# Performance work log

Hardware: AMD Instinct MI355X
Metric: run time of the kernel (lower is better)

The kernel has to match this reference:

```python
import jax, jax.numpy as jnp
import numpy as np


def setup_inputs() -> dict:
    key = jax.random.key(0)
    ks = jax.random.split(key, 20)
    B, P, ENC = 128, 196, 512
    DEC, ATT, EMB, V, S1 = 512, 256, 256, 5000, 257
    s = 0.02
    inp = {
        "features": jax.random.normal(ks[0], (B, P, ENC), jnp.float32),
        "captions": jax.random.randint(ks[1], (B, S1), 0, V),
        "emb": jax.random.normal(ks[2], (V, EMB), jnp.float32) * s,
        "Ua_w": jax.random.normal(ks[3], (ENC, ATT), jnp.float32) * s,
        "Ua_b": jnp.zeros((ATT,), jnp.float32),
        "Wa_w": jax.random.normal(ks[4], (DEC, ATT), jnp.float32) * s,
        "Wa_b": jnp.zeros((ATT,), jnp.float32),
        "va_w": jax.random.normal(ks[5], (ATT,), jnp.float32) * s,
        "va_b": jnp.zeros((), jnp.float32),
        "ih_w": jax.random.normal(ks[6], (ENC, DEC), jnp.float32) * s,
        "ih_b": jnp.zeros((DEC,), jnp.float32),
        "ic_w": jax.random.normal(ks[7], (ENC, DEC), jnp.float32) * s,
        "ic_b": jnp.zeros((DEC,), jnp.float32),
        "W_ih": jax.random.normal(ks[8], (EMB + ENC, 4 * DEC), jnp.float32) * s,
        "b_ih": jnp.zeros((4 * DEC,), jnp.float32),
        "W_hh": jax.random.normal(ks[9], (DEC, 4 * DEC), jnp.float32) * s,
        "b_hh": jnp.zeros((4 * DEC,), jnp.float32),
        "fcn_w": jax.random.normal(ks[10], (DEC, V), jnp.float32) * s,
        "fcn_b": jnp.zeros((V,), jnp.float32),
    }
    return inp


def reference(features, captions, emb, Ua_w, Ua_b, Wa_w, Wa_b, va_w, va_b,
              ih_w, ih_b, ic_w, ic_b, W_ih, b_ih, W_hh, b_hh, fcn_w, fcn_b):
    # embeds: [B, S+1, E]; we consume embeds[:, :S]
    embeds = emb[captions]
    mean_f = features.mean(axis=1)                      # [B, ENC]
    h0 = mean_f @ ih_w + ih_b                           # [B, DEC]
    c0 = mean_f @ ic_w + ic_b
    Uf = features @ Ua_w + Ua_b                         # [B, P, ATT] precomputed

    def step(carry, x_emb):
        h, c = carry
        att = jnp.tanh(Uf + (h @ Wa_w + Wa_b)[:, None, :])   # [B, P, ATT]
        scores = att @ va_w + va_b                            # [B, P]
        alpha = jax.nn.softmax(scores, axis=1)
        context = jnp.einsum('bp,bpe->be', alpha, features)   # [B, ENC]
        x = jnp.concatenate([x_emb, context], axis=1)         # [B, EMB+ENC]
        gates = x @ W_ih + b_ih + h @ W_hh + b_hh             # [B, 4*DEC]
        i, f, g, o = jnp.split(gates, 4, axis=1)
        c = jax.nn.sigmoid(f) * c + jax.nn.sigmoid(i) * jnp.tanh(g)
        h = jax.nn.sigmoid(o) * jnp.tanh(c)
        out = h @ fcn_w + fcn_b                               # dropout is identity (p=0)
        return (h, c), out

    xs = jnp.swapaxes(embeds[:, :-1], 0, 1)             # [S, B, EMB]
    _, preds = jax.lax.scan(step, (h0, c0), xs)         # [S, B, V]
    return jnp.swapaxes(preds, 0, 1)                    # [B, S, V]
```

## Files before the change

kernel.cpp:

```cpp
#include <hip/hip_runtime.h>
#include <hip/hip_bf16.h>

#define B 128
#define P 196
#define PP 200
#define ENC 512
#define DEC 512
#define ATT 256
#define EMB 256
#define V 5000
#define S 256
#define S1 257
#define NG 2048
#define KS 16

typedef __attribute__((ext_vector_type(4))) short s4v;
typedef __attribute__((ext_vector_type(8))) short s8v;

__device__ __forceinline__ float bf2f(short u) {
    unsigned int x = ((unsigned int)(unsigned short)u) << 16;
    float f; __builtin_memcpy(&f, &x, 4); return f;
}

__device__ __forceinline__ float tanhf_fast(float x) {
    float xx = fminf(fmaxf(x, -15.f), 15.f);
    float t = __expf(2.f * xx);
    return (t - 1.f) * __builtin_amdgcn_rcpf(t + 1.f);
}

__global__ __launch_bounds__(256) void k_mean(const float* __restrict__ feat,
                                              float* __restrict__ mean_f) {
    int idx = blockIdx.x * 256 + threadIdx.x;
    int b = idx >> 9, e = idx & 511;
    const float* fp = feat + (size_t)b * P * ENC + e;
    float s = 0.f;
    for (int p = 0; p < P; ++p) s += fp[(size_t)p * ENC];
    mean_f[idx] = s * (1.0f / (float)P);
}

__global__ __launch_bounds__(256) void k_init_hc(const float* __restrict__ mean_f,
        const float* __restrict__ ih_w, const float* __restrict__ ih_b,
        const float* __restrict__ ic_w, const float* __restrict__ ic_b,
        float* __restrict__ h, float* __restrict__ c) {
    int idx = blockIdx.x * 256 + threadIdx.x;
    int b = idx >> 9, d = idx & 511;
    const float* mf = mean_f + (size_t)b * ENC;
    float sh = ih_b[d], sc = ic_b[d];
    for (int e = 0; e < ENC; ++e) {
        float m = mf[e];
        sh = fmaf(m, ih_w[(size_t)e * DEC + d], sh);
        sc = fmaf(m, ic_w[(size_t)e * DEC + d], sc);
    }
    h[idx] = sh; c[idx] = sc;
}

__global__ __launch_bounds__(256) void k_uf(const float* __restrict__ feat,
        const float* __restrict__ Ua_w, const float* __restrict__ Ua_b,
        __hip_bfloat16* __restrict__ Uf) {
    int row0 = blockIdx.x * 8;
    int a = threadIdx.x;
    __shared__ float fs[8][ENC];
    for (int i = threadIdx.x; i < 8 * ENC; i += 256) {
        int r = i >> 9, e = i & 511;
        fs[r][e] = feat[(size_t)(row0 + r) * ENC + e];
    }
    __syncthreads();
    float acc[8];
    float bia = Ua_b[a];
#pragma unroll
    for (int r = 0; r < 8; ++r) acc[r] = bia;
    for (int e = 0; e < ENC; ++e) {
        float w = Ua_w[(size_t)e * ATT + a];
#pragma unroll
        for (int r = 0; r < 8; ++r) acc[r] = fmaf(fs[r][e], w, acc[r]);
    }
#pragma unroll
    for (int r = 0; r < 8; ++r)
        Uf[(size_t)(row0 + r) * ATT + a] = __float2bfloat16(acc[r]);
}

__global__ __launch_bounds__(512) void k_featT(const float* __restrict__ feat,
        __hip_bfloat16* __restrict__ featT) {
    int b = blockIdx.x, p0 = blockIdx.y * 8;
    int e = threadIdx.x;
    __hip_bfloat16 v[8];
#pragma unroll
    for (int i = 0; i < 8; ++i) {
        int p = p0 + i;
        float f = (p < P) ? feat[((size_t)b * P + p) * ENC + e] : 0.f;
        v[i] = __float2bfloat16(f);
    }
    __builtin_memcpy(&featT[((size_t)b * ENC + e) * PP + p0], v, 16);
}

__global__ __launch_bounds__(256) void k_wacvt(const float* __restrict__ w,
        __hip_bfloat16* __restrict__ wb) {
    int i = blockIdx.x * 256 + threadIdx.x;
    wb[i] = __float2bfloat16(w[i]);
}

__global__ __launch_bounds__(256) void k_gemb(const float* __restrict__ emb,
        const int* __restrict__ captions, const float* __restrict__ W_ih,
        __hip_bfloat16* __restrict__ Gemb) {
    __shared__ float As[16][128];
    __shared__ float Bs[16][128];
    __shared__ int rowcap[128];
    int m0 = blockIdx.x * 128;
    int n0 = blockIdx.y * 128;
    int tid = threadIdx.x;
    if (tid < 128) {
        int m = m0 + tid;
        rowcap[tid] = captions[(size_t)(m & 127) * S1 + (m >> 7)];
    }
    __syncthreads();
    int tx = tid & 15, ty = tid >> 4;
    float acc[8][8];
#pragma unroll
    for (int i = 0; i < 8; ++i)
#pragma unroll
        for (int j = 0; j < 8; ++j) acc[i][j] = 0.f;
    int arow = tid >> 1, ak = (tid & 1) * 8;
    int bkk = tid >> 4, bn = (tid & 15) * 8;
    for (int k0 = 0; k0 < EMB; k0 += 16) {
        {
            const float* ap = emb + (size_t)rowcap[arow] * EMB + k0 + ak;
            float4 v0 = *(const float4*)ap;
            float4 v1 = *(const float4*)(ap + 4);
            As[ak + 0][arow] = v0.x; As[ak + 1][arow] = v0.y;
            As[ak + 2][arow] = v0.z; As[ak + 3][arow] = v0.w;
            As[ak + 4][arow] = v1.x; As[ak + 5][arow] = v1.y;
            As[ak + 6][arow] = v1.z; As[ak + 7][arow] = v1.w;
        }
        {
            const float* bp = W_ih + (size_t)(k0 + bkk) * NG + n0 + bn;
            *(float4*)&Bs[bkk][bn] = *(const float4*)bp;
            *(float4*)&Bs[bkk][bn + 4] = *(const float4*)(bp + 4);
        }
        __syncthreads();
#pragma unroll
        for (int kk = 0; kk < 16; ++kk) {
            float4 a0 = *(const float4*)&As[kk][ty * 8];
            float4 a1 = *(const float4*)&As[kk][ty * 8 + 4];
            float4 b0 = *(const float4*)&Bs[kk][tx * 8];
            float4 b1 = *(const float4*)&Bs[kk][tx * 8 + 4];
            float av[8] = {a0.x, a0.y, a0.z, a0.w, a1.x, a1.y, a1.z, a1.w};
            float bv[8] = {b0.x, b0.y, b0.z, b0.w, b1.x, b1.y, b1.z, b1.w};
#pragma unroll
            for (int i = 0; i < 8; ++i)
#pragma unroll
                for (int j = 0; j < 8; ++j)
                    acc[i][j] = fmaf(av[i], bv[j], acc[i][j]);
        }
        __syncthreads();
    }
#pragma unroll
    for (int i = 0; i < 8; ++i) {
        __hip_bfloat16* gp = Gemb + (size_t)(m0 + ty * 8 + i) * NG + n0 + tx * 8;
#pragma unroll
        for (int j = 0; j < 8; ++j) gp[j] = __float2bfloat16(acc[i][j]);
    }
}

__global__ __launch_bounds__(1024) void k_attn_cell(
        const float* __restrict__ partials, const __hip_bfloat16* __restrict__ Gemb,
        const float* __restrict__ b_ih, const float* __restrict__ b_hh,
        float* __restrict__ h, const float* __restrict__ cr, float* __restrict__ cw,
        float* __restrict__ Hall,
        const __hip_bfloat16* __restrict__ Wa_wb, const float* __restrict__ Wa_b,
        const __hip_bfloat16* __restrict__ Uf, const __hip_bfloat16* __restrict__ featT,
        const float* __restrict__ va_w, const float* __restrict__ va_b,
        float* __restrict__ ctxp, float* __restrict__ mlp,
        int t, int use_gemb, int use_hall) {
    int g = blockIdx.x;
    int b = g >> 1, half = g & 1;
    int tid = threadIdx.x;
    int base = half ? 96 : 0;
    int cnt  = half ? 100 : 96;
    __shared__ short ufs[100][ATT];
    __shared__ float hs[DEC];
    __shared__ float wahp[4][ATT];
    __shared__ float wahs[ATT];
    __shared__ float sc[104];
    __shared__ float red[4];
    __shared__ float cpart[2][ENC];

    if (tid < 512) {
        if (t > 0) {
            int d = tid;
            float s0 = b_ih[d]           + b_hh[d];
            float s1 = b_ih[d + DEC]     + b_hh[d + DEC];
            float s2 = b_ih[d + 2 * DEC] + b_hh[d + 2 * DEC];
            float s3 = b_ih[d + 3 * DEC] + b_hh[d + 3 * DEC];
#pragma unroll
            for (int ks = 0; ks < KS; ++ks) {
                const float* pp = partials + ((size_t)ks * B + b) * NG + d;
                s0 += pp[0]; s1 += pp[DEC]; s2 += pp[2 * DEC]; s3 += pp[3 * DEC];
            }
            if (use_gemb) {
                const __hip_bfloat16* gp = Gemb + ((size_t)(t - 1) * B + b) * NG + d;
                s0 += __bfloat162float(gp[0]);
                s1 += __bfloat162float(gp[DEC]);
                s2 += __bfloat162float(gp[2 * DEC]);
                s3 += __bfloat162float(gp[3 * DEC]);
            }
            size_t gidx = (size_t)b * DEC + d;
            float ii = 1.f / (1.f + __expf(-s0));
            float ff = 1.f / (1.f + __expf(-s1));
            float gg = tanhf_fast(s2);
            float oo = 1.f / (1.f + __expf(-s3));
            float cn = ff * cr[gidx] + ii * gg;
            float hn = oo * tanhf_fast(cn);
            hs[d] = hn;
            if (half == 0) {
                cw[gidx] = cn;
                h[gidx] = hn;
                if (use_hall) Hall[((size_t)(t - 1) * B + b) * DEC + d] = hn;
            }
        } else {
            hs[tid] = h[(size_t)b * DEC + tid];
        }
    } else if (t < S) {
        const __hip_bfloat16* ub = Uf + ((size_t)b * P + base) * ATT;
        for (int i = tid - 512; i < cnt * 32; i += 512) {
            int p = i >> 5, c = (i & 31) * 8;
            *(s8v*)&ufs[p][c] = *(const s8v*)(ub + (size_t)p * ATT + c);
        }
    }
    __syncthreads();
    if (t == S) return;

    {
        int a = tid & 255, q = tid >> 8;
        float acc = 0.f;
        const __hip_bfloat16* wp = Wa_wb + (size_t)(q * 128) * ATT + a;
        const float* hq = &hs[q * 128];
#pragma unroll 4
        for (int dd = 0; dd < 128; ++dd)
            acc = fmaf(hq[dd], bf2f(*(const short*)&wp[(size_t)dd * ATT]), acc);
        wahp[q][a] = acc;
    }
    __syncthreads();
    if (tid < ATT)
        wahs[tid] = Wa_b[tid] + wahp[0][tid] + wahp[1][tid] + wahp[2][tid] + wahp[3][tid];
    __syncthreads();

    {
        int w = tid >> 6, lane = tid & 63;
        float4 wv = *(const float4*)&wahs[lane * 4];
        float4 vv = *(const float4*)&va_w[lane * 4];
        float vb = va_b[0];
        for (int pl = w; pl < cnt; pl += 16) {
            s4v u4 = *(const s4v*)&ufs[pl][lane * 4];
            float ssc = vv.x * tanhf_fast(bf2f(u4.x) + wv.x)
                      + vv.y * tanhf_fast(bf2f(u4.y) + wv.y)
                      + vv.z * tanhf_fast(bf2f(u4.z) + wv.z)
                      + vv.w * tanhf_fast(bf2f(u4.w) + wv.w);
#pragma unroll
            for (int off = 32; off; off >>= 1) ssc += __shfl_down(ssc, off);
            if (lane == 0) sc[pl] = ssc + vb;
        }
    }
    __syncthreads();

    {
        int lane = tid & 63;
        float v = (tid < cnt) ? sc[tid] : -1e30f;
        if (tid < 128) {
            float m = v;
#pragma unroll
            for (int off = 32; off; off >>= 1) m = fmaxf(m, __shfl_down(m, off));
            if (lane == 0) red[tid >> 6] = m;
        }
        __syncthreads();
        float mh = fmaxf(red[0], red[1]);
        float e = (tid < cnt) ? __expf(v - mh) : 0.f;
        if (tid < 128) {
            float l = e;
#pragma unroll
            for (int off = 32; off; off >>= 1) l += __shfl_down(l, off);
            if (lane == 0) red[2 + (tid >> 6)] = l;
        }
        __syncthreads();
        if (tid < cnt) sc[tid] = e;
        else if (tid < 104) sc[tid] = 0.f;
        if (tid == 0) {
            mlp[((size_t)half * B + b) * 2 + 0] = mh;
            mlp[((size_t)half * B + b) * 2 + 1] = red[2] + red[3];
        }
    }
    __syncthreads();

    {
        int e = tid & 511, ph = tid >> 9;
        int start = half ? (ph ? 7 : 0) : (ph ? 6 : 0);
        int nch   = half ? (ph ? 6 : 7) : 6;
        float acc = 0.f;
        const __hip_bfloat16* fr = featT + ((size_t)b * ENC + e) * PP + base + start * 8;
        for (int ch = 0; ch < nch; ++ch) {
            s8v raw = *(const s8v*)(fr + ch * 8);
            const float* sp = &sc[(start + ch) * 8];
#pragma unroll
            for (int j = 0; j < 8; ++j)
                acc = fmaf(sp[j], bf2f(raw[j]), acc);
        }
        cpart[ph][e] = acc;
    }
    __syncthreads();
    if (tid < ENC)
        ctxp[((size_t)half * B + b) * ENC + tid] = cpart[0][tid] + cpart[1][tid];
}

__global__ __launch_bounds__(256) void k_gates(const float* __restrict__ emb,
        const int* __restrict__ captions, int t,
        const float* __restrict__ ctxp, const float* __restrict__ mlp,
        const float* __restrict__ h,
        const float* __restrict__ W_ih, const float* __restrict__ W_hh,
        float* __restrict__ partials, int use_gemb) {
    __shared__ float As[2][16][128];
    __shared__ float Bs[2][16][64];
    __shared__ float sw0[B], sw1[B];
    __shared__ int scap[B];
    int n0 = blockIdx.x * 64;
    int ks = blockIdx.y;
    int tid = threadIdx.x;
    int kch = use_gemb ? 64 : 80;
    if (tid < B) {
        float m0 = mlp[(size_t)tid * 2 + 0];
        float l0 = mlp[(size_t)tid * 2 + 1];
        float m1 = mlp[((size_t)B + tid) * 2 + 0];
        float l1 = mlp[((size_t)B + tid) * 2 + 1];
        float M = fmaxf(m0, m1);
        float e0 = __expf(m0 - M), e1 = __expf(m1 - M);
        float inv = 1.f / (l0 * e0 + l1 * e1);
        sw0[tid] = e0 * inv; sw1[tid] = e1 * inv;
        if (!use_gemb) scap[tid] = captions[(size_t)tid * S1 + t];
    }
    int tx = tid & 15, ty = tid >> 4;
    float acc[8][4];
#pragma unroll
    for (int i = 0; i < 8; ++i)
#pragma unroll
        for (int j = 0; j < 4; ++j) acc[i][j] = 0.f;
    int arow = tid >> 1, ak = (tid & 1) * 8;
    int bkk = tid >> 4, bn = (tid & 15) * 4;
    int kbase = ks * kch;
    int nch = kch >> 4;
    float rA[8];
    float4 rB;
    __syncthreads();

    {
        int k = kbase + ak;
        if (!use_gemb && k < EMB) {
            const float* ap = emb + (size_t)scap[arow] * EMB + k;
            float4 v0 = *(const float4*)ap;
            float4 v1 = *(const float4*)(ap + 4);
            rA[0] = v0.x; rA[1] = v0.y; rA[2] = v0.z; rA[3] = v0.w;
            rA[4] = v1.x; rA[5] = v1.y; rA[6] = v1.z; rA[7] = v1.w;
        } else {
            int kc = use_gemb ? k : (k - EMB);
            if (kc < ENC) {
                const float* p0 = ctxp + (size_t)arow * ENC + kc;
                const float* p1 = ctxp + ((size_t)B + arow) * ENC + kc;
                float w0 = sw0[arow], w1 = sw1[arow];
                float4 a0 = *(const float4*)p0;
                float4 a1 = *(const float4*)(p0 + 4);
                float4 b0 = *(const float4*)p1;
                float4 b1 = *(const float4*)(p1 + 4);
                rA[0] = a0.x * w0 + b0.x * w1; rA[1] = a0.y * w0 + b0.y * w1;
                rA[2] = a0.z * w0 + b0.z * w1; rA[3] = a0.w * w0 + b0.w * w1;
                rA[4] = a1.x * w0 + b1.x * w1; rA[5] = a1.y * w0 + b1.y * w1;
                rA[6] = a1.z * w0 + b1.z * w1; rA[7] = a1.w * w0 + b1.w * w1;
            } else {
                const float* ap = h + (size_t)arow * DEC + (kc - ENC);
                float4 v0 = *(const float4*)ap;
                float4 v1 = *(const float4*)(ap + 4);
                rA[0] = v0.x; rA[1] = v0.y; rA[2] = v0.z; rA[3] = v0.w;
                rA[4] = v1.x; rA[5] = v1.y; rA[6] = v1.z; rA[7] = v1.w;
            }
        }
        int kb = kbase + bkk;
        const float* bp;
        if (use_gemb)
            bp = (kb < ENC) ? W_ih + (size_t)(kb + EMB) * NG + n0 + bn
                            : W_hh + (size_t)(kb - ENC) * NG + n0 + bn;
        else
            bp = (kb < EMB + ENC) ? W_ih + (size_t)kb * NG + n0 + bn
                                  : W_hh + (size_t)(kb - EMB - ENC) * NG + n0 + bn;
        rB = *(const float4*)bp;
    }
#pragma unroll
    for (int i = 0; i < 8; ++i) As[0][ak + i][arow] = rA[i];
    *(float4*)&Bs[0][bkk][bn] = rB;
    __syncthreads();

    for (int c = 0; c < nch; ++c) {
        int cur = c & 1;
        bool more = (c + 1 < nch);
        if (more) {
            int k0 = kbase + (c + 1) * 16;
            int k = k0 + ak;
            if (!use_gemb && k < EMB) {
                const float* ap = emb + (size_t)scap[arow] * EMB + k;
                float4 v0 = *(const float4*)ap;
                float4 v1 = *(const float4*)(ap + 4);
                rA[0] = v0.x; rA[1] = v0.y; rA[2] = v0.z; rA[3] = v0.w;
                rA[4] = v1.x; rA[5] = v1.y; rA[6] = v1.z; rA[7] = v1.w;
            } else {
                int kc = use_gemb ? k : (k - EMB);
                if (kc < ENC) {
                    const float* p0 = ctxp + (size_t)arow * ENC + kc;
                    const float* p1 = ctxp + ((size_t)B + arow) * ENC + kc;
                    float w0 = sw0[arow], w1 = sw1[arow];
                    float4 a0 = *(const float4*)p0;
                    float4 a1 = *(const float4*)(p0 + 4);
                    float4 b0 = *(const float4*)p1;
                    float4 b1 = *(const float4*)(p1 + 4);
                    rA[0] = a0.x * w0 + b0.x * w1; rA[1] = a0.y * w0 + b0.y * w1;
                    rA[2] = a0.z * w0 + b0.z * w1; rA[3] = a0.w * w0 + b0.w * w1;
                    rA[4] = a1.x * w0 + b1.x * w1; rA[5] = a1.y * w0 + b1.y * w1;
                    rA[6] = a1.z * w0 + b1.z * w1; rA[7] = a1.w * w0 + b1.w * w1;
                } else {
                    const float* ap = h + (size_t)arow * DEC + (kc - ENC);
                    float4 v0 = *(const float4*)ap;
                    float4 v1 = *(const float4*)(ap + 4);
                    rA[0] = v0.x; rA[1] = v0.y; rA[2] = v0.z; rA[3] = v0.w;
                    rA[4] = v1.x; rA[5] = v1.y; rA[6] = v1.z; rA[7] = v1.w;
                }
            }
            int kb = k0 + bkk;
            const float* bp;
            if (use_gemb)
                bp = (kb < ENC) ? W_ih + (size_t)(kb + EMB) * NG + n0 + bn
                                : W_hh + (size_t)(kb - ENC) * NG + n0 + bn;
            else
                bp = (kb < EMB + ENC) ? W_ih + (size_t)kb * NG + n0 + bn
                                      : W_hh + (size_t)(kb - EMB - ENC) * NG + n0 + bn;
            rB = *(const float4*)bp;
        }
#pragma unroll
        for (int kk = 0; kk < 16; ++kk) {
            float4 a0 = *(const float4*)&As[cur][kk][ty * 8];
            float4 a1 = *(const float4*)&As[cur][kk][ty * 8 + 4];
            float4 b0 = *(const float4*)&Bs[cur][kk][tx * 4];
            float av[8] = {a0.x, a0.y, a0.z, a0.w, a1.x, a1.y, a1.z, a1.w};
            float bv[4] = {b0.x, b0.y, b0.z, b0.w};
#pragma unroll
            for (int i = 0; i < 8; ++i)
#pragma unroll
                for (int j = 0; j < 4; ++j)
                    acc[i][j] = fmaf(av[i], bv[j], acc[i][j]);
        }
        if (more) {
#pragma unroll
            for (int i = 0; i < 8; ++i) As[cur ^ 1][ak + i][arow] = rA[i];
            *(float4*)&Bs[cur ^ 1][bkk][bn] = rB;
            __syncthreads();
        }
    }
#pragma unroll
    for (int i = 0; i < 8; ++i) {
        int mrow = ty * 8 + i;
        float* pp = partials + ((size_t)ks * B + mrow) * NG + n0 + tx * 4;
        *(float4*)pp = make_float4(acc[i][0], acc[i][1], acc[i][2], acc[i][3]);
    }
}

__global__ __launch_bounds__(256) void k_fcn(const float* __restrict__ A,
        const float* __restrict__ Bw, const float* __restrict__ bias,
        float* __restrict__ out, int t_fix) {
    __shared__ float As[16][128];
    __shared__ float Bs[16][128];
    int m0 = blockIdx.x * 128;
    int n0 = blockIdx.y * 128;
    int tid = threadIdx.x;
    int tx = tid & 15, ty = tid >> 4;
    float acc[8][8];
#pragma unroll
    for (int i = 0; i < 8; ++i)
#pragma unroll
        for (int j = 0; j < 8; ++j) acc[i][j] = 0.f;
    int arow = tid >> 1, ak = (tid & 1) * 8;
    int bkk = tid >> 4, bn = (tid & 15) * 8;
    const float4 z4 = make_float4(0.f, 0.f, 0.f, 0.f);
    for (int k0 = 0; k0 < DEC; k0 += 16) {
        {
            const float* ap = A + (size_t)(m0 + arow) * DEC + k0 + ak;
            float4 v0 = *(const float4*)ap;
            float4 v1 = *(const float4*)(ap + 4);
            As[ak + 0][arow] = v0.x; As[ak + 1][arow] = v0.y;
            As[ak + 2][arow] = v0.z; As[ak + 3][arow] = v0.w;
            As[ak + 4][arow] = v1.x; As[ak + 5][arow] = v1.y;
            As[ak + 6][arow] = v1.z; As[ak + 7][arow] = v1.w;
        }
        {
            int n4 = n0 + bn;
            const float* bp = Bw + (size_t)(k0 + bkk) * V + n4;
            float4 v0 = (n4 < V) ? *(const float4*)bp : z4;
            float4 v1 = (n4 + 4 < V) ? *(const float4*)(bp + 4) : z4;
            *(float4*)&Bs[bkk][bn] = v0;
            *(float4*)&Bs[bkk][bn + 4] = v1;
        }
        __syncthreads();
#pragma unroll
        for (int kk = 0; kk < 16; ++kk) {
            float4 a0 = *(const float4*)&As[kk][ty * 8];
            float4 a1 = *(const float4*)&As[kk][ty * 8 + 4];
            float4 b0 = *(const float4*)&Bs[kk][tx * 8];
            float4 b1 = *(const float4*)&Bs[kk][tx * 8 + 4];
            float av[8] = {a0.x, a0.y, a0.z, a0.w, a1.x, a1.y, a1.z, a1.w};
            float bv[8] = {b0.x, b0.y, b0.z, b0.w, b1.x, b1.y, b1.z, b1.w};
#pragma unroll
            for (int i = 0; i < 8; ++i)
#pragma unroll
                for (int j = 0; j < 8; ++j)
                    acc[i][j] = fmaf(av[i], bv[j], acc[i][j]);
        }
        __syncthreads();
    }
#pragma unroll
    for (int i = 0; i < 8; ++i) {
        int mrow = m0 + ty * 8 + i;
        int bb, tt;
        if (t_fix >= 0) { bb = mrow; tt = t_fix; }
        else            { tt = mrow >> 7; bb = mrow & 127; }
        float* op = out + ((size_t)bb * S + tt) * V + n0 + tx * 8;
#pragma unroll
        for (int j = 0; j < 8; ++j) {
            int n = n0 + tx * 8 + j;
            if (n < V) op[j] = acc[i][j] + bias[n];
        }
    }
}

extern "C" void kernel_launch(void* const* d_in, const int* in_sizes, int n_in,
                              void* d_out, int out_size, void* d_ws, size_t ws_size,
                              hipStream_t stream) {
    const float* features = (const float*)d_in[0];
    const int*   captions = (const int*)d_in[1];
    const float* emb      = (const float*)d_in[2];
    const float* Ua_w     = (const float*)d_in[3];
    const float* Ua_b     = (const float*)d_in[4];
    const float* Wa_w     = (const float*)d_in[5];
    const float* Wa_b     = (const float*)d_in[6];
    const float* va_w     = (const float*)d_in[7];
    const float* va_b     = (const float*)d_in[8];
    const float* ih_w     = (const float*)d_in[9];
    const float* ih_b     = (const float*)d_in[10];
    const float* ic_w     = (const float*)d_in[11];
    const float* ic_b     = (const float*)d_in[12];
    const float* W_ih     = (const float*)d_in[13];
    const float* b_ih     = (const float*)d_in[14];
    const float* W_hh     = (const float*)d_in[15];
    const float* b_hh     = (const float*)d_in[16];
    const float* fcn_w    = (const float*)d_in[17];
    const float* fcn_b    = (const float*)d_in[18];
    float* out = (float*)d_out;
    char* wsb  = (char*)d_ws;

    size_t off = 0;
    __hip_bfloat16* Uf    = (__hip_bfloat16*)(wsb + off); off += (size_t)B * P * ATT * 2;
    __hip_bfloat16* featT = (__hip_bfloat16*)(wsb + off); off += (size_t)B * ENC * PP * 2;
    __hip_bfloat16* Wa_wb = (__hip_bfloat16*)(wsb + off); off += (size_t)DEC * ATT * 2;
    float* partials = (float*)(wsb + off); off += (size_t)KS * B * NG * 4;
    float* hbuf     = (float*)(wsb + off); off += (size_t)B * DEC * 4;
    float* cbufA    = (float*)(wsb + off); off += (size_t)B * DEC * 4;
    float* cbufB    = (float*)(wsb + off); off += (size_t)B * DEC * 4;
    float* ctxp     = (float*)(wsb + off); off += (size_t)2 * B * ENC * 4;
    float* mlp      = (float*)(wsb + off); off += 4096;
    float* meanf    = ctxp;
    size_t need_min = off;
    float* Hall     = (float*)(wsb + off); off += (size_t)S * B * DEC * 4;
    size_t need_hall = off;
    __hip_bfloat16* Gemb = (__hip_bfloat16*)(wsb + off);
    off += (size_t)S * B * NG * 2;
    size_t need_gemb = off;

    (void)need_min;
    int use_hall = ws_size >= need_hall;
    int use_gemb = ws_size >= need_gemb;

    k_mean<<<256, 256, 0, stream>>>(features, meanf);
    k_init_hc<<<256, 256, 0, stream>>>(meanf, ih_w, ih_b, ic_w, ic_b, hbuf, cbufA);
    k_uf<<<3136, 256, 0, stream>>>(features, Ua_w, Ua_b, Uf);
    k_featT<<<dim3(128, 25), 512, 0, stream>>>(features, featT);
    k_wacvt<<<512, 256, 0, stream>>>(Wa_w, Wa_wb);
    if (use_gemb)
        k_gemb<<<dim3(256, 16), 256, 0, stream>>>(emb, captions, W_ih, Gemb);

    for (int t = 0; t <= S; ++t) {
        const float* crd = (t & 1) ? cbufA : cbufB;
        float*       cwr = (t & 1) ? cbufB : cbufA;
        k_attn_cell<<<256, 1024, 0, stream>>>(partials, Gemb, b_ih, b_hh,
                hbuf, crd, cwr, Hall, Wa_wb, Wa_b, Uf, featT, va_w, va_b,
                ctxp, mlp, t, use_gemb, use_hall);
        if (t < S)
            k_gates<<<dim3(32, KS), 256, 0, stream>>>(emb, captions, t, ctxp, mlp,
                    hbuf, W_ih, W_hh, partials, use_gemb);
        if (!use_hall && t > 0)
            k_fcn<<<dim3(1, 40), 256, 0, stream>>>(hbuf, fcn_w, fcn_b, out, t - 1);
    }
    if (use_hall)
        k_fcn<<<dim3(256, 40), 256, 0, stream>>>(Hall, fcn_w, fcn_b, out, -1);
}
```

Measured before the change: 14.11 ms.

## Use split-bf16 MFMA for final vocab projection and transpose attention weights

The final batched FC projection over all hidden states is moved from an fp32 SIMT GEMM to bf16 MFMA using a hi/lo split (three MFMAs per tile) to keep near-fp32 accuracy. Hidden states are stored as bf16 hi/lo pairs, and the fcn weights are transposed and split in a new prep kernel that reuses the Uf workspace after the recurrence finishes. Separately, Wa_w is stored transposed so each thread reads contiguous 8-wide vectors in the per-step Wa·h product instead of strided scalar loads. The split adds work and small precision risk, and aliasing the Uf workspace relies on ordering within the stream.

```diff
diff --git a/kernel.cpp b/kernel.cpp
--- a/kernel.cpp
+++ b/kernel.cpp
@@ -9,13 +9,16 @@
 #define ATT 256
 #define EMB 256
 #define V 5000
+#define NP 5120
 #define S 256
 #define S1 257
 #define NG 2048
 #define KS 16
+#define KTP 40
 
 typedef __attribute__((ext_vector_type(4))) short s4v;
 typedef __attribute__((ext_vector_type(8))) short s8v;
+typedef __attribute__((ext_vector_type(4))) float f32x4;
 
 __device__ __forceinline__ float bf2f(short u) {
     unsigned int x = ((unsigned int)(unsigned short)u) << 16;
@@ -93,10 +96,11 @@
     __builtin_memcpy(&featT[((size_t)b * ENC + e) * PP + p0], v, 16);
 }
 
-__global__ __launch_bounds__(256) void k_wacvt(const float* __restrict__ w,
-        __hip_bfloat16* __restrict__ wb) {
+__global__ __launch_bounds__(256) void k_watr(const float* __restrict__ w,
+        __hip_bfloat16* __restrict__ wT) {
     int i = blockIdx.x * 256 + threadIdx.x;
-    wb[i] = __float2bfloat16(w[i]);
+    int d = i >> 8, a = i & 255;
+    wT[(size_t)a * DEC + d] = __float2bfloat16(w[i]);
 }
 
 __global__ __launch_bounds__(256) void k_gemb(const float* __restrict__ emb,
@@ -165,8 +169,8 @@
         const float* __restrict__ partials, const __hip_bfloat16* __restrict__ Gemb,
         const float* __restrict__ b_ih, const float* __restrict__ b_hh,
         float* __restrict__ h, const float* __restrict__ cr, float* __restrict__ cw,
-        float* __restrict__ Hall,
-        const __hip_bfloat16* __restrict__ Wa_wb, const float* __restrict__ Wa_b,
+        __hip_bfloat16* __restrict__ HallH, __hip_bfloat16* __restrict__ HallL,
+        const __hip_bfloat16* __restrict__ WaT, const float* __restrict__ Wa_b,
         const __hip_bfloat16* __restrict__ Uf, const __hip_bfloat16* __restrict__ featT,
         const float* __restrict__ va_w, const float* __restrict__ va_b,
         float* __restrict__ ctxp, float* __restrict__ mlp,
@@ -214,7 +218,13 @@
             if (half == 0) {
                 cw[gidx] = cn;
                 h[gidx] = hn;
-                if (use_hall) Hall[((size_t)(t - 1) * B + b) * DEC + d] = hn;
+                if (use_hall) {
+                    __hip_bfloat16 hi = __float2bfloat16(hn);
+                    float lo = hn - __bfloat162float(hi);
+                    size_t hidx = ((size_t)(t - 1) * B + b) * DEC + d;
+                    HallH[hidx] = hi;
+                    HallL[hidx] = __float2bfloat16(lo);
+                }
             }
         } else {
             hs[tid] = h[(size_t)b * DEC + tid];
@@ -231,12 +241,16 @@
 
     {
         int a = tid & 255, q = tid >> 8;
+        const __hip_bfloat16* wp = WaT + (size_t)a * DEC + q * 128;
         float acc = 0.f;
-        const __hip_bfloat16* wp = Wa_wb + (size_t)(q * 128) * ATT + a;
-        const float* hq = &hs[q * 128];
-#pragma unroll 4
-        for (int dd = 0; dd < 128; ++dd)
-            acc = fmaf(hq[dd], bf2f(*(const short*)&wp[(size_t)dd * ATT]), acc);
+#pragma unroll
+        for (int c = 0; c < 16; ++c) {
+            s8v w8 = *(const s8v*)(wp + c * 8);
+            const float* hq = &hs[q * 128 + c * 8];
+#pragma unroll
+            for (int j = 0; j < 8; ++j)
+                acc = fmaf(hq[j], bf2f(w8[j]), acc);
+        }
         wahp[q][a] = acc;
     }
     __syncthreads();
@@ -466,6 +480,103 @@
     }
 }
 
+__global__ __launch_bounds__(256) void k_wsplit(const float* __restrict__ w,
+        __hip_bfloat16* __restrict__ WhiT, __hip_bfloat16* __restrict__ WloT) {
+    __shared__ float ls[32][65];
+    int k0 = blockIdx.x * 32;
+    int n0 = blockIdx.y * 64;
+    int tid = threadIdx.x;
+    for (int idx = tid; idx < 32 * 64; idx += 256) {
+        int kk = idx >> 6, nn = idx & 63;
+        int n = n0 + nn;
+        ls[kk][nn] = (n < V) ? w[(size_t)(k0 + kk) * V + n] : 0.f;
+    }
+    __syncthreads();
+    for (int idx = tid; idx < 64 * 32; idx += 256) {
+        int nn = idx >> 5, kk = idx & 31;
+        float x = ls[kk][nn];
+        __hip_bfloat16 hi = __float2bfloat16(x);
+        float lo = x - __bfloat162float(hi);
+        size_t o = (size_t)(n0 + nn) * 512 + k0 + kk;
+        WhiT[o] = hi;
+        WloT[o] = __float2bfloat16(lo);
+    }
+}
+
+__global__ __launch_bounds__(256) void k_fcn_mfma(
+        const __hip_bfloat16* __restrict__ Ahi, const __hip_bfloat16* __restrict__ Alo,
+        const __hip_bfloat16* __restrict__ WhiT, const __hip_bfloat16* __restrict__ WloT,
+        const float* __restrict__ bias, float* __restrict__ out) {
+    __shared__ short AsH[128][KTP], AsL[128][KTP];
+    __shared__ short BsH[128][KTP], BsL[128][KTP];
+    int m0 = blockIdx.x * 128;
+    int n0 = blockIdx.y * 128;
+    int tid = threadIdx.x;
+    int wid = tid >> 6, lane = tid & 63;
+    int wr = wid >> 1, wc = wid & 1;
+    f32x4 acc[4][4] = {};
+    int r = tid & 127;
+    const __hip_bfloat16* asrc = (tid < 128 ? Ahi : Alo) + (size_t)(m0 + r) * 512;
+    const __hip_bfloat16* bsrc = (tid < 128 ? WhiT : WloT) + (size_t)(n0 + r) * 512;
+    short* adst = (tid < 128 ? &AsH[r][0] : &AsL[r][0]);
+    short* bdst = (tid < 128 ? &BsH[r][0] : &BsL[r][0]);
+    int l15 = lane & 15, kof = (lane >> 4) * 8;
+
+    for (int k0 = 0; k0 < 512; k0 += 32) {
+        {
+            const __hip_bfloat16* s = asrc + k0;
+            *(s8v*)(adst + 0)  = *(const s8v*)(s + 0);
+            *(s8v*)(adst + 8)  = *(const s8v*)(s + 8);
+            *(s8v*)(adst + 16) = *(const s8v*)(s + 16);
+            *(s8v*)(adst + 24) = *(const s8v*)(s + 24);
+            const __hip_bfloat16* sb = bsrc + k0;
+            *(s8v*)(bdst + 0)  = *(const s8v*)(sb + 0);
+            *(s8v*)(bdst + 8)  = *(const s8v*)(sb + 8);
+            *(s8v*)(bdst + 16) = *(const s8v*)(sb + 16);
+            *(s8v*)(bdst + 24) = *(const s8v*)(sb + 24);
+        }
+        __syncthreads();
+        s8v ah[4], al[4], bh[4], bl[4];
+#pragma unroll
+        for (int mi = 0; mi < 4; ++mi) {
+            int row = wr * 64 + mi * 16 + l15;
+            ah[mi] = *(const s8v*)&AsH[row][kof];
+            al[mi] = *(const s8v*)&AsL[row][kof];
+        }
+#pragma unroll
+        for (int ni = 0; ni < 4; ++ni) {
+            int row = wc * 64 + ni * 16 + l15;
+            bh[ni] = *(const s8v*)&BsH[row][kof];
+            bl[ni] = *(const s8v*)&BsL[row][kof];
+        }
+#pragma unroll
+        for (int mi = 0; mi < 4; ++mi)
+#pragma unroll
+            for (int ni = 0; ni < 4; ++ni) {
+                acc[mi][ni] = __builtin_amdgcn_mfma_f32_16x16x32_bf16(ah[mi], bh[ni], acc[mi][ni], 0, 0, 0);
+                acc[mi][ni] = __builtin_amdgcn_mfma_f32_16x16x32_bf16(ah[mi], bl[ni], acc[mi][ni], 0, 0, 0);
+                acc[mi][ni] = __builtin_amdgcn_mfma_f32_16x16x32_bf16(al[mi], bh[ni], acc[mi][ni], 0, 0, 0);
+            }
+        __syncthreads();
+    }
+#pragma unroll
+    for (int ni = 0; ni < 4; ++ni) {
+        int col = n0 + wc * 64 + ni * 16 + l15;
+        if (col >= V) continue;
+        float bv = bias[col];
+#pragma unroll
+        for (int mi = 0; mi < 4; ++mi) {
+            int rbase = m0 + wr * 64 + mi * 16 + (lane >> 4) * 4;
+#pragma unroll
+            for (int j = 0; j < 4; ++j) {
+                int m = rbase + j;
+                int tt = m >> 7, bb = m & 127;
+                out[((size_t)bb * S + tt) * V + col] = acc[mi][ni][j] + bv;
+            }
+        }
+    }
+}
+
 __global__ __launch_bounds__(256) void k_fcn(const float* __restrict__ A,
         const float* __restrict__ Bw, const float* __restrict__ bias,
         float* __restrict__ out, int t_fix) {
@@ -521,9 +632,7 @@
 #pragma unroll
     for (int i = 0; i < 8; ++i) {
         int mrow = m0 + ty * 8 + i;
-        int bb, tt;
-        if (t_fix >= 0) { bb = mrow; tt = t_fix; }
-        else            { tt = mrow >> 7; bb = mrow & 127; }
+        int bb = mrow, tt = t_fix;
         float* op = out + ((size_t)bb * S + tt) * V + n0 + tx * 8;
 #pragma unroll
         for (int j = 0; j < 8; ++j) {
@@ -561,7 +670,7 @@
     size_t off = 0;
     __hip_bfloat16* Uf    = (__hip_bfloat16*)(wsb + off); off += (size_t)B * P * ATT * 2;
     __hip_bfloat16* featT = (__hip_bfloat16*)(wsb + off); off += (size_t)B * ENC * PP * 2;
-    __hip_bfloat16* Wa_wb = (__hip_bfloat16*)(wsb + off); off += (size_t)DEC * ATT * 2;
+    __hip_bfloat16* WaT   = (__hip_bfloat16*)(wsb + off); off += (size_t)ATT * DEC * 2;
     float* partials = (float*)(wsb + off); off += (size_t)KS * B * NG * 4;
     float* hbuf     = (float*)(wsb + off); off += (size_t)B * DEC * 4;
     float* cbufA    = (float*)(wsb + off); off += (size_t)B * DEC * 4;
@@ -570,11 +679,14 @@
     float* mlp      = (float*)(wsb + off); off += 4096;
     float* meanf    = ctxp;
     size_t need_min = off;
-    float* Hall     = (float*)(wsb + off); off += (size_t)S * B * DEC * 4;
+    __hip_bfloat16* HallH = (__hip_bfloat16*)(wsb + off); off += (size_t)S * B * DEC * 2;
+    __hip_bfloat16* HallL = (__hip_bfloat16*)(wsb + off); off += (size_t)S * B * DEC * 2;
     size_t need_hall = off;
     __hip_bfloat16* Gemb = (__hip_bfloat16*)(wsb + off);
     off += (size_t)S * B * NG * 2;
     size_t need_gemb = off;
+    __hip_bfloat16* WhiT = (__hip_bfloat16*)Uf;
+    __hip_bfloat16* WloT = WhiT + (size_t)NP * 512;
 
     (void)need_min;
     int use_hall = ws_size >= need_hall;
@@ -584,7 +696,7 @@
     k_init_hc<<<256, 256, 0, stream>>>(meanf, ih_w, ih_b, ic_w, ic_b, hbuf, cbufA);
     k_uf<<<3136, 256, 0, stream>>>(features, Ua_w, Ua_b, Uf);
     k_featT<<<dim3(128, 25), 512, 0, stream>>>(features, featT);
-    k_wacvt<<<512, 256, 0, stream>>>(Wa_w, Wa_wb);
+    k_watr<<<512, 256, 0, stream>>>(Wa_w, WaT);
     if (use_gemb)
         k_gemb<<<dim3(256, 16), 256, 0, stream>>>(emb, captions, W_ih, Gemb);
 
@@ -592,7 +704,7 @@
         const float* crd = (t & 1) ? cbufA : cbufB;
         float*       cwr = (t & 1) ? cbufB : cbufA;
         k_attn_cell<<<256, 1024, 0, stream>>>(partials, Gemb, b_ih, b_hh,
-                hbuf, crd, cwr, Hall, Wa_wb, Wa_b, Uf, featT, va_w, va_b,
+                hbuf, crd, cwr, HallH, HallL, WaT, Wa_b, Uf, featT, va_w, va_b,
                 ctxp, mlp, t, use_gemb, use_hall);
         if (t < S)
             k_gates<<<dim3(32, KS), 256, 0, stream>>>(emb, captions, t, ctxp, mlp,
@@ -600,6 +712,8 @@
         if (!use_hall && t > 0)
             k_fcn<<<dim3(1, 40), 256, 0, stream>>>(hbuf, fcn_w, fcn_b, out, t - 1);
     }
-    if (use_hall)
-        k_fcn<<<dim3(256, 40), 256, 0, stream>>>(Hall, fcn_w, fcn_b, out, -1);
-}
+    if (use_hall) {
+        k_wsplit<<<dim3(16, 80), 256, 0, stream>>>(fcn_w, WhiT, WloT);
+        k_fcn_mfma<<<dim3(256, 40), 256, 0, stream>>>(HallH, HallL, WhiT, WloT, fcn_b, out);
+    }
+}
```

Result: faster. 13.03 ms (-7.6%).
